# Kernel optimization log

Hardware: AMD Instinct MI355X
Metric: run time of the kernel (lower is better)

Reference implementation:

```python
import jax, jax.numpy as jnp
import numpy as np

COMMITMENT_COST = 0.25
NUM_EMBEDDINGS = 4096
EMBEDDING_DIM = 256
INPUT_DIM = 1024


def setup_inputs() -> dict:
    key = jax.random.key(0)
    k1, k2, k3, k4 = jax.random.split(key, 4)
    B, T = 16, 2048
    features = jax.random.normal(k1, (B, T, INPUT_DIM), dtype=jnp.float32)
    # Linear params (torch default init scale ~ 1/sqrt(fan_in))
    W = jax.random.normal(k2, (EMBEDDING_DIM, INPUT_DIM), dtype=jnp.float32) / np.sqrt(INPUT_DIM)
    b = jax.random.normal(k3, (EMBEDDING_DIM,), dtype=jnp.float32) * 0.01
    # Codebook: uniform(-1/K, 1/K) as in the torch module
    codebook = jax.random.uniform(
        k4, (NUM_EMBEDDINGS, EMBEDDING_DIM), dtype=jnp.float32,
        minval=-1.0 / NUM_EMBEDDINGS, maxval=1.0 / NUM_EMBEDDINGS)
    return {"features": features, "W": W, "b": b, "codebook": codebook}


def reference(features, W, b, codebook):
    B, T, _ = features.shape
    # encoder projection: [B,T,input_dim] @ [input_dim,embed_dim]
    proj = jnp.einsum('btc,dc->btd', features, W) + b  # [B,T,D]
    flat = proj.reshape(-1, EMBEDDING_DIM)             # [N,D]
    # squared L2 distances to codebook via expansion
    distances = (jnp.sum(flat * flat, axis=1, keepdims=True)
                 + jnp.sum(codebook * codebook, axis=1)
                 - 2.0 * flat @ codebook.T)            # [N,K]
    indices = jnp.argmin(distances, axis=1)            # [N]
    quantized = codebook[indices].reshape(B, T, EMBEDDING_DIM)
    e_latent_loss = jnp.mean((jax.lax.stop_gradient(quantized) - proj) ** 2)
    q_latent_loss = jnp.mean((quantized - jax.lax.stop_gradient(proj)) ** 2)
    loss = q_latent_loss + COMMITMENT_COST * e_latent_loss
    # straight-through estimator
    quantized_ste = proj + jax.lax.stop_gradient(quantized - proj)
    return quantized_ste, loss, indices.reshape(B, T)
```

## Files before the change

kernel.cpp:

```cpp
#include <hip/hip_runtime.h>


typedef _Float16 f16;
typedef _Float16 half8 __attribute__((ext_vector_type(8)));
typedef float floatx4 __attribute__((ext_vector_type(4)));

#define ROWS   32768
#define IN_DIM 1024
#define DDIM   256
#define KEMB   4096
#define TAU    0.125f
#define RSB    8
#define ERB    8

__device__ __forceinline__ float fmul(float a, float b) { return __fmul_rn(a, b); }
__device__ __forceinline__ float fadd(float a, float b) { return __fadd_rn(a, b); }

__device__ __forceinline__ void split2(float x, f16& hi, f16& lo) {
    float h = (float)(f16)x;
    if (__builtin_fabsf(h) < 6.1035156e-5f) h = 0.0f;
    hi = (f16)h;
    lo = (f16)((x - h) * 2048.0f);
}

__device__ float np_sumsq_256(const float* __restrict__ x) {
    float blk[2];
    #pragma unroll
    for (int h = 0; h < 2; ++h) {
        const float* p = x + h * 128;
        float s[16];
        #pragma unroll
        for (int l = 0; l < 16; ++l) {
            float q0 = fmul(p[l],       p[l]);
            float q1 = fmul(p[16 + l],  p[16 + l]);
            float q2 = fmul(p[32 + l],  p[32 + l]);
            float q3 = fmul(p[48 + l],  p[48 + l]);
            float q4 = fmul(p[64 + l],  p[64 + l]);
            float q5 = fmul(p[80 + l],  p[80 + l]);
            float q6 = fmul(p[96 + l],  p[96 + l]);
            float q7 = fmul(p[112 + l], p[112 + l]);
            s[l] = fadd(fadd(fadd(q0, q1), fadd(q2, q3)),
                        fadd(fadd(q4, q5), fadd(q6, q7)));
        }
        float t1[8];
        #pragma unroll
        for (int l = 0; l < 8; ++l) t1[l] = fadd(s[l], s[l + 8]);
        float t2[4];
        #pragma unroll
        for (int l = 0; l < 4; ++l) t2[l] = fadd(t1[l], t1[l + 4]);
        blk[h] = fadd(fadd(t2[0], t2[2]), fadd(t2[1], t2[3]));
    }
    return fadd(blk[0], blk[1]);
}

__global__ __launch_bounds__(256) void vq_transpose_w(
    const float* __restrict__ Wm, float* __restrict__ WT)
{
    __shared__ float t[64][65];
    const int d0 = blockIdx.x * 64, k0 = blockIdx.y * 64;
    const int tid = threadIdx.x;
    for (int e = tid; e < 4096; e += 256) {
        int dr = e >> 6, kc = e & 63;
        t[dr][kc] = Wm[(size_t)(d0 + dr) * IN_DIM + k0 + kc];
    }
    __syncthreads();
    for (int e = tid; e < 4096; e += 256) {
        int kr = e >> 6, dc = e & 63;
        WT[(size_t)(k0 + kr) * DDIM + d0 + dc] = t[dc][kr];
    }
}

__global__ __launch_bounds__(256) void vq_prep_codebook(
    const float* __restrict__ cb, f16* __restrict__ chiF, float* __restrict__ cn3)
{
    int j = blockIdx.x;
    int d = threadIdx.x;
    float c = cb[(size_t)j * DDIM + d] * 4096.0f;
    f16 hi, lo;
    split2(c, hi, lo);
    chiF[((size_t)(j >> 4) * 32 + (d >> 3)) * 128 + (size_t)(j & 15) * 8 + (d & 7)] = hi;
    float sq = c * c;
    #pragma unroll
    for (int off = 32; off > 0; off >>= 1) sq += __shfl_down(sq, off);
    __shared__ float red[4];
    if ((threadIdx.x & 63) == 0) red[threadIdx.x >> 6] = sq;
    __syncthreads();
    if (threadIdx.x == 0)
        cn3[j] = (red[0] + red[1] + red[2] + red[3]) * (1.0f / 8192.0f);
}

__global__ __launch_bounds__(256) void vq_proj_mfma(
    const float* __restrict__ feat, const float* __restrict__ Wm,
    const float* __restrict__ bias, float* __restrict__ pf, f16* __restrict__ phi)
{
    __shared__ f16 FH[128][40], WH[64][40], WL[64][40];
    const int m0 = blockIdx.x * 128;
    const int n0 = blockIdx.y * 64;
    const int tid = threadIdx.x;
    const int lane = tid & 63;
    const int w = tid >> 6;
    const int wr = w >> 1, wc = w & 1;

    floatx4 acc1[4][2], acc2[4][2];
    #pragma unroll
    for (int mi = 0; mi < 4; ++mi)
        #pragma unroll
        for (int ni = 0; ni < 2; ++ni) {
            acc1[mi][ni] = (floatx4){0.f, 0.f, 0.f, 0.f};
            acc2[mi][ni] = (floatx4){0.f, 0.f, 0.f, 0.f};
        }

    for (int kt = 0; kt < IN_DIM / 32; ++kt) {
        {
            int r = tid >> 1, h = (tid & 1) * 16;
            const float* src = feat + (size_t)(m0 + r) * IN_DIM + kt * 32 + h;
            f16 th[16];
            #pragma unroll
            for (int i = 0; i < 16; i += 4) {
                float4 v = *(const float4*)(src + i);
                th[i+0] = (f16)v.x;
                th[i+1] = (f16)v.y;
                th[i+2] = (f16)v.z;
                th[i+3] = (f16)v.w;
            }
            *(half8*)&FH[r][h]     = *(half8*)&th[0];
            *(half8*)&FH[r][h + 8] = *(half8*)&th[8];
        }
        {
            int c = tid >> 2, q = (tid & 3) * 8;
            const float* src = Wm + (size_t)(n0 + c) * IN_DIM + kt * 32 + q;
            f16 th[8], tl[8];
            #pragma unroll
            for (int i = 0; i < 8; i += 4) {
                float4 v = *(const float4*)(src + i);
                split2(v.x, th[i+0], tl[i+0]);
                split2(v.y, th[i+1], tl[i+1]);
                split2(v.z, th[i+2], tl[i+2]);
                split2(v.w, th[i+3], tl[i+3]);
            }
            *(half8*)&WH[c][q] = *(half8*)&th[0];
            *(half8*)&WL[c][q] = *(half8*)&tl[0];
        }
        __syncthreads();

        const int k8 = (lane >> 4) * 8;
        const int l15 = lane & 15;
        half8 aH[4], bH[2], bL[2];
        #pragma unroll
        for (int mi = 0; mi < 4; ++mi) {
            int r = wr * 64 + mi * 16 + l15;
            aH[mi] = *(half8*)&FH[r][k8];
        }
        #pragma unroll
        for (int ni = 0; ni < 2; ++ni) {
            int c = wc * 32 + ni * 16 + l15;
            bH[ni] = *(half8*)&WH[c][k8];
            bL[ni] = *(half8*)&WL[c][k8];
        }
        #pragma unroll
        for (int mi = 0; mi < 4; ++mi)
            #pragma unroll
            for (int ni = 0; ni < 2; ++ni) {
                acc1[mi][ni] = __builtin_amdgcn_mfma_f32_16x16x32_f16(aH[mi], bH[ni], acc1[mi][ni], 0, 0, 0);
                acc2[mi][ni] = __builtin_amdgcn_mfma_f32_16x16x32_f16(aH[mi], bL[ni], acc2[mi][ni], 0, 0, 0);
            }
        __syncthreads();
    }

    #pragma unroll
    for (int ni = 0; ni < 2; ++ni) {
        int col = n0 + wc * 32 + ni * 16 + (lane & 15);
        float bv = bias[col];
        #pragma unroll
        for (int mi = 0; mi < 4; ++mi) {
            #pragma unroll
            for (int j = 0; j < 4; ++j) {
                int row = m0 + wr * 64 + mi * 16 + (lane >> 4) * 4 + j;
                float p = acc1[mi][ni][j] + acc2[mi][ni][j] * (1.0f / 2048.0f) + bv;
                pf[(size_t)row * DDIM + col] = p;
                f16 hi, dead;
                split2(p, hi, dead);
                phi[(size_t)row * DDIM + col] = hi;
            }
        }
    }
}

__global__ __launch_bounds__(256) void vq_argmin(
    const f16* __restrict__ phi,
    const f16* __restrict__ chiF,
    const float* __restrict__ cn3,
    int* __restrict__ out_idx,
    int* __restrict__ fs_cnt, int* __restrict__ fs_list)
{
    __shared__ float mV1[64][2], mV2[64][2];
    __shared__ int   mI1[64][2];
    const int m0 = blockIdx.x * 64;
    const int tid = threadIdx.x;
    const int lane = tid & 63;
    const int w = tid >> 6;
    const int wr = w >> 1, wc = w & 1;
    const int l15 = lane & 15;
    const int lhi = lane >> 4;

    half8 aH[2][8];
    #pragma unroll
    for (int mi = 0; mi < 2; ++mi) {
        const int row = m0 + wr * 32 + mi * 16 + l15;
        #pragma unroll
        for (int t = 0; t < 8; ++t)
            aH[mi][t] = *(const half8*)&phi[(size_t)row * DDIM + t * 32 + lhi * 8];
    }

    float v1s[8], v2s[8];
    int i1s[8];
    #pragma unroll
    for (int s = 0; s < 8; ++s) { v1s[s] = -__builtin_inff(); v2s[s] = -__builtin_inff(); i1s[s] = 0; }

    for (int nt = 0; nt < KEMB / 128; ++nt) {
        floatx4 acc1[2][4];
        #pragma unroll
        for (int mi = 0; mi < 2; ++mi)
            #pragma unroll
            for (int ni = 0; ni < 4; ++ni)
                acc1[mi][ni] = (floatx4){0.f, 0.f, 0.f, 0.f};

        #pragma unroll
        for (int ks = 0; ks < 4; ++ks) {
            #pragma unroll
            for (int kb = 0; kb < 2; ++kb) {
                const int t = ks * 8 + kb * 4 + lhi;
                half8 bH[4];
                #pragma unroll
                for (int ni = 0; ni < 4; ++ni) {
                    const int c16 = nt * 8 + wc * 4 + ni;
                    bH[ni] = *(const half8*)&chiF[((size_t)c16 * 32 + t) * 128 + (size_t)l15 * 8];
                }
                #pragma unroll
                for (int mi = 0; mi < 2; ++mi)
                    #pragma unroll
                    for (int ni = 0; ni < 4; ++ni)
                        acc1[mi][ni] = __builtin_amdgcn_mfma_f32_16x16x32_f16(aH[mi][ks * 2 + kb], bH[ni], acc1[mi][ni], 0, 0, 0);
            }
        }

        const int colbase = nt * 128 + wc * 64 + l15;
        float cn0 = cn3[colbase];
        float cn1 = cn3[colbase + 16];
        float cn2 = cn3[colbase + 32];
        float cn3v = cn3[colbase + 48];
        #pragma unroll
        for (int mi = 0; mi < 2; ++mi)
            #pragma unroll
            for (int j = 0; j < 4; ++j) {
                const int s = mi * 4 + j;
                float x0 = acc1[mi][0][j] - cn0;
                float x1 = acc1[mi][1][j] - cn1;
                float x2 = acc1[mi][2][j] - cn2;
                float x3 = acc1[mi][3][j] - cn3v;
                float mx = fmaxf(fmaxf(x0, x1), fmaxf(x2, x3));
                if (mx > v1s[s]) {
                    int nidx; float rest;
                    if (x0 == mx)      { nidx = 0; rest = fmaxf(fmaxf(x1, x2), x3); }
                    else if (x1 == mx) { nidx = 1; rest = fmaxf(fmaxf(x0, x2), x3); }
                    else if (x2 == mx) { nidx = 2; rest = fmaxf(fmaxf(x0, x1), x3); }
                    else               { nidx = 3; rest = fmaxf(fmaxf(x0, x1), x2); }
                    v2s[s] = fmaxf(v1s[s], rest);
                    v1s[s] = mx;
                    i1s[s] = colbase + nidx * 16;
                } else {
                    v2s[s] = fmaxf(v2s[s], mx);
                }
            }
    }

    #pragma unroll
    for (int s = 0; s < 8; ++s) {
        float a1 = v1s[s], a2 = v2s[s];
        int ai = i1s[s];
        #pragma unroll
        for (int m = 1; m < 16; m <<= 1) {
            float b1 = __shfl_xor(a1, m);
            float b2 = __shfl_xor(a2, m);
            int   bi = __shfl_xor(ai, m);
            float n2 = fmaxf(fminf(a1, b1), fmaxf(a2, b2));
            if (b1 > a1 || (b1 == a1 && bi < ai)) { a1 = b1; ai = bi; }
            a2 = n2;
        }
        v1s[s] = a1; v2s[s] = a2; i1s[s] = ai;
    }
    if (l15 == 0) {
        #pragma unroll
        for (int s = 0; s < 8; ++s) {
            int mi = s >> 2, j = s & 3;
            int rloc = wr * 32 + mi * 16 + lhi * 4 + j;
            mV1[rloc][wc] = v1s[s]; mV2[rloc][wc] = v2s[s];
            mI1[rloc][wc] = i1s[s];
        }
    }
    __syncthreads();
    if (tid < 64) {
        float a1 = mV1[tid][0], a2 = mV2[tid][0], b1 = mV1[tid][1], b2 = mV2[tid][1];
        int ai = mI1[tid][0], bi = mI1[tid][1];
        float n2 = fmaxf(fminf(a1, b1), fmaxf(a2, b2));
        if (b1 > a1 || (b1 == a1 && bi < ai)) { a1 = b1; ai = bi; }
        out_idx[m0 + tid] = ai;
        if (a1 - n2 < TAU) {
            int slot = atomicAdd(fs_cnt, 1);
            fs_list[slot] = m0 + tid;
        }
    }
}

__global__ __launch_bounds__(256) void vq_transpose_cb(
    const float* __restrict__ cb, float* __restrict__ cbT)
{
    __shared__ float t[64][65];
    const int j0 = blockIdx.x * 64, d0 = blockIdx.y * 64;
    const int tid = threadIdx.x;
    for (int e = tid; e < 4096; e += 256) {
        int jr = e >> 6, dc = e & 63;
        t[jr][dc] = cb[(size_t)(j0 + jr) * DDIM + d0 + dc];
    }
    __syncthreads();
    for (int e = tid; e < 4096; e += 256) {
        int dr = e >> 6, jc = e & 63;
        cbT[(size_t)(d0 + dr) * KEMB + j0 + jc] = t[jc][dr];
    }
}

__global__ __launch_bounds__(256) void vq_proj_exact_rows(
    const float* __restrict__ feat, const float* __restrict__ WT,
    const float* __restrict__ bias, const int* __restrict__ fs_list,
    const int* __restrict__ fs_cnt, float* __restrict__ pf)
{
    const int d = threadIdx.x;
    int cnt = *fs_cnt;
    if (cnt > ROWS) cnt = ROWS;
    for (int base = blockIdx.x * ERB; base < cnt; base += gridDim.x * ERB) {
        const int nr = min(ERB, cnt - base);
        int rows[ERB];
        #pragma unroll
        for (int r = 0; r < ERB; ++r)
            rows[r] = fs_list[base + ((r < nr) ? r : (nr - 1))];

        float acc[ERB][4];
        #pragma unroll
        for (int r = 0; r < ERB; ++r)
            #pragma unroll
            for (int l = 0; l < 4; ++l)
                acc[r][l] = 0.0f;

        #pragma unroll 1
        for (int ch = 0; ch < IN_DIM / 16; ++ch) {
            const int ko = ch * 16;
            float wk[16];
            #pragma unroll
            for (int k = 0; k < 16; ++k)
                wk[k] = WT[(size_t)(ko + k) * DDIM + d];
            #pragma unroll
            for (int r = 0; r < ERB; ++r) {
                const float* fr = feat + (size_t)rows[r] * IN_DIM + ko;
                float4 f3 = *(const float4*)(fr + 12);
                float4 f2 = *(const float4*)(fr + 8);
                float4 f1 = *(const float4*)(fr + 4);
                float4 f0 = *(const float4*)(fr);
                acc[r][0] = fadd(acc[r][0], fmul(f3.x, wk[12]));
                acc[r][1] = fadd(acc[r][1], fmul(f3.y, wk[13]));
                acc[r][2] = fadd(acc[r][2], fmul(f3.z, wk[14]));
                acc[r][3] = fadd(acc[r][3], fmul(f3.w, wk[15]));
                acc[r][0] = fadd(acc[r][0], fmul(f2.x, wk[8]));
                acc[r][1] = fadd(acc[r][1], fmul(f2.y, wk[9]));
                acc[r][2] = fadd(acc[r][2], fmul(f2.z, wk[10]));
                acc[r][3] = fadd(acc[r][3], fmul(f2.w, wk[11]));
                acc[r][0] = fadd(acc[r][0], fmul(f1.x, wk[4]));
                acc[r][1] = fadd(acc[r][1], fmul(f1.y, wk[5]));
                acc[r][2] = fadd(acc[r][2], fmul(f1.z, wk[6]));
                acc[r][3] = fadd(acc[r][3], fmul(f1.w, wk[7]));
                acc[r][0] = fadd(acc[r][0], fmul(f0.x, wk[0]));
                acc[r][1] = fadd(acc[r][1], fmul(f0.y, wk[1]));
                acc[r][2] = fadd(acc[r][2], fmul(f0.z, wk[2]));
                acc[r][3] = fadd(acc[r][3], fmul(f0.w, wk[3]));
            }
        }

        const float bv = bias[d];
        for (int r = 0; r < nr; ++r) {
            float h = fadd(fadd(acc[r][0], acc[r][1]), fadd(acc[r][2], acc[r][3]));
            pf[(size_t)rows[r] * DDIM + d] = fadd(h, bv);
        }
    }
}

__global__ __launch_bounds__(256) void vq_np_rescan(
    const float* __restrict__ pf, const float* __restrict__ cbT,
    const int* __restrict__ fs_list, const int* __restrict__ fs_cnt,
    int* __restrict__ out_idx)
{
    __shared__ float prow[RSB][DDIM];
    __shared__ float As[RSB];
    __shared__ float rD[RSB][4];
    __shared__ int   rJ[RSB][4];
    const int tid = threadIdx.x;
    const int lane = tid & 63;
    const int wv = tid >> 6;
    int cnt = *fs_cnt;
    if (cnt > ROWS) cnt = ROWS;

    for (int base = blockIdx.x * RSB; base < cnt; base += gridDim.x * RSB) {
        const int nr = min(RSB, cnt - base);
        __syncthreads();
        for (int i = tid; i < nr * 64; i += 256) {
            int r = i >> 6, q = (i & 63) * 4;
            *(float4*)&prow[r][q] =
                *(const float4*)&pf[(size_t)fs_list[base + r] * DDIM + q];
        }
        __syncthreads();
        if (tid < nr) As[tid] = np_sumsq_256(prow[tid]);
        __syncthreads();

        float bD[RSB]; int bJ[RSB];
        #pragma unroll
        for (int r = 0; r < RSB; ++r) { bD[r] = __builtin_inff(); bJ[r] = 0x7fffffff; }

        for (int sw = 0; sw < 4; ++sw) {
            const int j0 = sw * 1024 + tid * 4;
            float4 acc[RSB];
            #pragma unroll
            for (int r = 0; r < RSB; ++r) acc[r] = (float4){0.f, 0.f, 0.f, 0.f};
            for (int d4 = 0; d4 < DDIM / 4; ++d4) {
                float4 pv[RSB];
                #pragma unroll
                for (int r = 0; r < RSB; ++r)
                    pv[r] = *(const float4*)&prow[r][d4 * 4];
                #pragma unroll
                for (int dd = 0; dd < 4; ++dd) {
                    float4 cv = *(const float4*)&cbT[(size_t)(d4 * 4 + dd) * KEMB + j0];
                    #pragma unroll
                    for (int r = 0; r < RSB; ++r) {
                        float p = (dd == 0) ? pv[r].x : (dd == 1) ? pv[r].y
                                 : (dd == 2) ? pv[r].z : pv[r].w;
                        acc[r].x = __fmaf_rn(p, cv.x, acc[r].x);
                        acc[r].y = __fmaf_rn(p, cv.y, acc[r].y);
                        acc[r].z = __fmaf_rn(p, cv.z, acc[r].z);
                        acc[r].w = __fmaf_rn(p, cv.w, acc[r].w);
                    }
                }
            }
            #pragma unroll
            for (int r = 0; r < RSB; ++r) {
                float A = As[r];
                float D0 = fadd(A, fmul(-2.0f, acc[r].x));
                float D1 = fadd(A, fmul(-2.0f, acc[r].y));
                float D2 = fadd(A, fmul(-2.0f, acc[r].z));
                float D3 = fadd(A, fmul(-2.0f, acc[r].w));
                if (D0 < bD[r]) { bD[r] = D0; bJ[r] = j0; }
                if (D1 < bD[r]) { bD[r] = D1; bJ[r] = j0 + 1; }
                if (D2 < bD[r]) { bD[r] = D2; bJ[r] = j0 + 2; }
                if (D3 < bD[r]) { bD[r] = D3; bJ[r] = j0 + 3; }
            }
        }

        #pragma unroll
        for (int r = 0; r < RSB; ++r) {
            float d_ = bD[r]; int j_ = bJ[r];
            #pragma unroll
            for (int m = 1; m < 64; m <<= 1) {
                float od = __shfl_xor(d_, m);
                int   oj = __shfl_xor(j_, m);
                if (od < d_ || (od == d_ && oj < j_)) { d_ = od; j_ = oj; }
            }
            if (lane == 0) { rD[r][wv] = d_; rJ[r][wv] = j_; }
        }
        __syncthreads();
        if (tid < nr) {
            float d_ = rD[tid][0]; int j_ = rJ[tid][0];
            #pragma unroll
            for (int q = 1; q < 4; ++q) {
                float od = rD[tid][q]; int oj = rJ[tid][q];
                if (od < d_ || (od == d_ && oj < j_)) { d_ = od; j_ = oj; }
            }
            out_idx[fs_list[base + tid]] = j_;
        }
    }
}

__global__ __launch_bounds__(256) void vq_gather(
    const float* __restrict__ cb, const float* __restrict__ pf,
    const int* __restrict__ idx,
    float* __restrict__ out0, float* __restrict__ outIdxF,
    float* __restrict__ partials)
{
    const int tid = threadIdx.x;
    const int lane = tid & 63;
    const int w = tid >> 6;
    const int row = blockIdx.x * 4 + w;
    const int k = idx[row];

    float4 c = *(const float4*)&cb[(size_t)k * DDIM + lane * 4];
    float4 p = *(const float4*)&pf[(size_t)row * DDIM + lane * 4];
    float d0 = c.x - p.x, d1 = c.y - p.y, d2 = c.z - p.z, d3 = c.w - p.w;
    float s = d0 * d0 + d1 * d1 + d2 * d2 + d3 * d3;

    *(float4*)&out0[(size_t)row * DDIM + lane * 4] = c;
    if (lane == 0) outIdxF[row] = (float)k;

    #pragma unroll
    for (int off = 32; off > 0; off >>= 1) s += __shfl_down(s, off);
    __shared__ float red[4];
    if (lane == 0) red[w] = s;
    __syncthreads();
    if (tid == 0) partials[blockIdx.x] = red[0] + red[1] + red[2] + red[3];
}

__global__ __launch_bounds__(256) void vq_loss(
    const float* __restrict__ partials, float* __restrict__ out_loss)
{
    const int tid = threadIdx.x;
    float s = 0.f;
    for (int i = tid; i < ROWS / 4; i += 256) s += partials[i];
    #pragma unroll
    for (int off = 32; off > 0; off >>= 1) s += __shfl_down(s, off);
    __shared__ float red[4];
    if ((tid & 63) == 0) red[tid >> 6] = s;
    __syncthreads();
    if (tid == 0)
        out_loss[0] = 1.25f * (red[0] + red[1] + red[2] + red[3]) / 8388608.0f;
}

extern "C" void kernel_launch(void* const* d_in, const int* in_sizes, int n_in,
                              void* d_out, int out_size, void* d_ws, size_t ws_size,
                              hipStream_t stream) {
    const float* feat = (const float*)d_in[0];
    const float* Wm   = (const float*)d_in[1];
    const float* bias = (const float*)d_in[2];
    const float* cb   = (const float*)d_in[3];

    char* ws = (char*)d_ws;
    float* pf       = (float*)(ws);
    f16*   chiF     = (f16*)(ws + 33554432);
    float* cbT      = (float*)(ws + 33554432);
    float* cn3      = (float*)(ws + 37748736);
    int*   idx      = (int*)(ws + 37765120);
    float* partials = (float*)(ws + 37896192);
    int*   fs_cnt   = (int*)(ws + 37928960);
    int*   fs_list  = (int*)(ws + 37929088);
    float* WT       = (float*)(ws + 38076416);
    f16*   phi      = (f16*)(ws + 39124992);

    float* out0    = (float*)d_out;
    float* outLoss = (float*)d_out + 8388608;
    float* outIdxF = (float*)d_out + 8388609;

    hipMemsetAsync(fs_cnt, 0, 4, stream);
    vq_transpose_w<<<dim3(DDIM / 64, IN_DIM / 64), 256, 0, stream>>>(Wm, WT);
    vq_prep_codebook<<<KEMB, 256, 0, stream>>>(cb, chiF, cn3);
    vq_proj_mfma<<<dim3(ROWS / 128, DDIM / 64), 256, 0, stream>>>(feat, Wm, bias, pf, phi);
    vq_argmin<<<ROWS / 64, 256, 0, stream>>>(phi, chiF, cn3, idx, fs_cnt, fs_list);
    vq_transpose_cb<<<dim3(KEMB / 64, DDIM / 64), 256, 0, stream>>>(cb, cbT);
    vq_proj_exact_rows<<<256, 256, 0, stream>>>(feat, WT, bias, fs_list, fs_cnt, pf);
    vq_np_rescan<<<512, 256, 0, stream>>>(pf, cbT, fs_list, fs_cnt, idx);
    vq_gather<<<ROWS / 4, 256, 0, stream>>>(cb, pf, idx, out0, outIdxF, partials);
    vq_loss<<<1, 256, 0, stream>>>(partials, outLoss);
}
```

Before: 440.2 us.

## Split argmin over codebook halves with merge kernel; widen projection N-tile

The argmin kernel now runs over two halves of the codebook in a 2D grid, writing per-split best, second-best and index to workspace, and a new merge kernel combines them and builds the near-tie list. The projection GEMM tile grows from 64 to 128 columns, so the feature matrix is read and converted to half precision half as often. The argmin split adds parallelism (1024 blocks instead of 512) at the cost of an extra launch and intermediate traffic. The wider projection tile raises register and LDS use per block, which may lower occupancy.

```diff
diff --git a/kernel.cpp b/kernel.cpp
--- a/kernel.cpp
+++ b/kernel.cpp
@@ -12,6 +12,8 @@
 #define TAU    0.125f
 #define RSB    8
 #define ERB    8
+#define NSPLIT 2
+#define NTPER  16
 
 __device__ __forceinline__ float fmul(float a, float b) { return __fmul_rn(a, b); }
 __device__ __forceinline__ float fadd(float a, float b) { return __fadd_rn(a, b); }
@@ -93,19 +95,21 @@
     const float* __restrict__ feat, const float* __restrict__ Wm,
     const float* __restrict__ bias, float* __restrict__ pf, f16* __restrict__ phi)
 {
-    __shared__ f16 FH[128][40], WH[64][40], WL[64][40];
+    __shared__ f16 FH[128][40], WH[128][40], WL[128][40];
     const int m0 = blockIdx.x * 128;
-    const int n0 = blockIdx.y * 64;
+    const int n0 = blockIdx.y * 128;
     const int tid = threadIdx.x;
     const int lane = tid & 63;
     const int w = tid >> 6;
     const int wr = w >> 1, wc = w & 1;
-
-    floatx4 acc1[4][2], acc2[4][2];
+    const int l15 = lane & 15;
+    const int lhi = lane >> 4;
+
+    floatx4 acc1[4][4], acc2[4][4];
     #pragma unroll
     for (int mi = 0; mi < 4; ++mi)
         #pragma unroll
-        for (int ni = 0; ni < 2; ++ni) {
+        for (int ni = 0; ni < 4; ++ni) {
             acc1[mi][ni] = (floatx4){0.f, 0.f, 0.f, 0.f};
             acc2[mi][ni] = (floatx4){0.f, 0.f, 0.f, 0.f};
         }
@@ -127,40 +131,41 @@
             *(half8*)&FH[r][h + 8] = *(half8*)&th[8];
         }
         {
-            int c = tid >> 2, q = (tid & 3) * 8;
+            int c = tid >> 1, q = (tid & 1) * 16;
             const float* src = Wm + (size_t)(n0 + c) * IN_DIM + kt * 32 + q;
-            f16 th[8], tl[8];
-            #pragma unroll
-            for (int i = 0; i < 8; i += 4) {
+            f16 th[16], tl[16];
+            #pragma unroll
+            for (int i = 0; i < 16; i += 4) {
                 float4 v = *(const float4*)(src + i);
                 split2(v.x, th[i+0], tl[i+0]);
                 split2(v.y, th[i+1], tl[i+1]);
                 split2(v.z, th[i+2], tl[i+2]);
                 split2(v.w, th[i+3], tl[i+3]);
             }
-            *(half8*)&WH[c][q] = *(half8*)&th[0];
-            *(half8*)&WL[c][q] = *(half8*)&tl[0];
+            *(half8*)&WH[c][q]     = *(half8*)&th[0];
+            *(half8*)&WH[c][q + 8] = *(half8*)&th[8];
+            *(half8*)&WL[c][q]     = *(half8*)&tl[0];
+            *(half8*)&WL[c][q + 8] = *(half8*)&tl[8];
         }
         __syncthreads();
 
-        const int k8 = (lane >> 4) * 8;
-        const int l15 = lane & 15;
-        half8 aH[4], bH[2], bL[2];
+        const int k8 = lhi * 8;
+        half8 aH[4], bH[4], bL[4];
         #pragma unroll
         for (int mi = 0; mi < 4; ++mi) {
             int r = wr * 64 + mi * 16 + l15;
             aH[mi] = *(half8*)&FH[r][k8];
         }
         #pragma unroll
-        for (int ni = 0; ni < 2; ++ni) {
-            int c = wc * 32 + ni * 16 + l15;
+        for (int ni = 0; ni < 4; ++ni) {
+            int c = wc * 64 + ni * 16 + l15;
             bH[ni] = *(half8*)&WH[c][k8];
             bL[ni] = *(half8*)&WL[c][k8];
         }
         #pragma unroll
         for (int mi = 0; mi < 4; ++mi)
             #pragma unroll
-            for (int ni = 0; ni < 2; ++ni) {
+            for (int ni = 0; ni < 4; ++ni) {
                 acc1[mi][ni] = __builtin_amdgcn_mfma_f32_16x16x32_f16(aH[mi], bH[ni], acc1[mi][ni], 0, 0, 0);
                 acc2[mi][ni] = __builtin_amdgcn_mfma_f32_16x16x32_f16(aH[mi], bL[ni], acc2[mi][ni], 0, 0, 0);
             }
@@ -168,14 +173,14 @@
     }
 
     #pragma unroll
-    for (int ni = 0; ni < 2; ++ni) {
-        int col = n0 + wc * 32 + ni * 16 + (lane & 15);
+    for (int ni = 0; ni < 4; ++ni) {
+        int col = n0 + wc * 64 + ni * 16 + l15;
         float bv = bias[col];
         #pragma unroll
         for (int mi = 0; mi < 4; ++mi) {
             #pragma unroll
             for (int j = 0; j < 4; ++j) {
-                int row = m0 + wr * 64 + mi * 16 + (lane >> 4) * 4 + j;
+                int row = m0 + wr * 64 + mi * 16 + lhi * 4 + j;
                 float p = acc1[mi][ni][j] + acc2[mi][ni][j] * (1.0f / 2048.0f) + bv;
                 pf[(size_t)row * DDIM + col] = p;
                 f16 hi, dead;
@@ -190,12 +195,12 @@
     const f16* __restrict__ phi,
     const f16* __restrict__ chiF,
     const float* __restrict__ cn3,
-    int* __restrict__ out_idx,
-    int* __restrict__ fs_cnt, int* __restrict__ fs_list)
+    float* __restrict__ tV1, float* __restrict__ tV2, int* __restrict__ tI1)
 {
     __shared__ float mV1[64][2], mV2[64][2];
     __shared__ int   mI1[64][2];
     const int m0 = blockIdx.x * 64;
+    const int split = blockIdx.y;
     const int tid = threadIdx.x;
     const int lane = tid & 63;
     const int w = tid >> 6;
@@ -217,7 +222,8 @@
     #pragma unroll
     for (int s = 0; s < 8; ++s) { v1s[s] = -__builtin_inff(); v2s[s] = -__builtin_inff(); i1s[s] = 0; }
 
-    for (int nt = 0; nt < KEMB / 128; ++nt) {
+    const int nt0 = split * NTPER;
+    for (int nt = nt0; nt < nt0 + NTPER; ++nt) {
         floatx4 acc1[2][4];
         #pragma unroll
         for (int mi = 0; mi < 2; ++mi)
@@ -304,11 +310,35 @@
         int ai = mI1[tid][0], bi = mI1[tid][1];
         float n2 = fmaxf(fminf(a1, b1), fmaxf(a2, b2));
         if (b1 > a1 || (b1 == a1 && bi < ai)) { a1 = b1; ai = bi; }
-        out_idx[m0 + tid] = ai;
-        if (a1 - n2 < TAU) {
-            int slot = atomicAdd(fs_cnt, 1);
-            fs_list[slot] = m0 + tid;
-        }
+        size_t o = (size_t)split * ROWS + m0 + tid;
+        tV1[o] = a1; tV2[o] = n2; tI1[o] = ai;
+    }
+}
+
+__global__ __launch_bounds__(256) void vq_merge(
+    const float* __restrict__ tV1, const float* __restrict__ tV2,
+    const int* __restrict__ tI1, int* __restrict__ out_idx,
+    int* __restrict__ fs_cnt, int* __restrict__ fs_list)
+{
+    const int row = blockIdx.x * 256 + threadIdx.x;
+    float a1 = tV1[row], a2 = tV2[row];
+    int ai = tI1[row];
+    #pragma unroll
+    for (int s = 1; s < NSPLIT; ++s) {
+        size_t o = (size_t)s * ROWS + row;
+        float b1 = tV1[o], b2 = tV2[o];
+        int bi = tI1[o];
+        if (b1 > a1 || (b1 == a1 && bi < ai)) {
+            a2 = fmaxf(a1, b2);
+            a1 = b1; ai = bi;
+        } else {
+            a2 = fmaxf(a2, b1);
+        }
+    }
+    out_idx[row] = ai;
+    if (a1 - a2 < TAU) {
+        int slot = atomicAdd(fs_cnt, 1);
+        fs_list[slot] = row;
     }
 }
 
@@ -540,6 +570,9 @@
     float* pf       = (float*)(ws);
     f16*   chiF     = (f16*)(ws + 33554432);
     float* cbT      = (float*)(ws + 33554432);
+    float* tV1      = (float*)(ws + 35651584);
+    float* tV2      = (float*)(ws + 35913728);
+    int*   tI1      = (int*)(ws + 36175872);
     float* cn3      = (float*)(ws + 37748736);
     int*   idx      = (int*)(ws + 37765120);
     float* partials = (float*)(ws + 37896192);
@@ -555,8 +588,9 @@
     hipMemsetAsync(fs_cnt, 0, 4, stream);
     vq_transpose_w<<<dim3(DDIM / 64, IN_DIM / 64), 256, 0, stream>>>(Wm, WT);
     vq_prep_codebook<<<KEMB, 256, 0, stream>>>(cb, chiF, cn3);
-    vq_proj_mfma<<<dim3(ROWS / 128, DDIM / 64), 256, 0, stream>>>(feat, Wm, bias, pf, phi);
-    vq_argmin<<<ROWS / 64, 256, 0, stream>>>(phi, chiF, cn3, idx, fs_cnt, fs_list);
+    vq_proj_mfma<<<dim3(ROWS / 128, DDIM / 128), 256, 0, stream>>>(feat, Wm, bias, pf, phi);
+    vq_argmin<<<dim3(ROWS / 64, NSPLIT), 256, 0, stream>>>(phi, chiF, cn3, tV1, tV2, tI1);
+    vq_merge<<<ROWS / 256, 256, 0, stream>>>(tV1, tV2, tI1, idx, fs_cnt, fs_list);
     vq_transpose_cb<<<dim3(KEMB / 64, DDIM / 64), 256, 0, stream>>>(cb, cbT);
     vq_proj_exact_rows<<<256, 256, 0, stream>>>(feat, WT, bias, fs_list, fs_cnt, pf);
     vq_np_rescan<<<512, 256, 0, stream>>>(pf, cbT, fs_list, fs_cnt, idx);
```

Result: slower. 499.7 us (+13.5%).
